# Optimization experiments

Measured on AMD Instinct MI355X. Metric: run time of the kernel, lower is better.

## Reference

```python
import jax, jax.numpy as jnp
import numpy as np

H, S, B, R, IN, NN, OP = 512, 256, 32, 16, 4, 16, 6
NEG = -1.0e12


def setup_inputs() -> dict:
    key = jax.random.key(0)
    ks = jax.random.split(key, 40)
    f32 = jnp.float32
    inp = {}
    inp["node_emb"] = jax.random.normal(ks[0], (B, 1, H), f32)
    inp["left"] = jax.random.normal(ks[1], (B, 1, H), f32)
    inp["encoder_outputs"] = jax.random.normal(ks[2], (S, B, H), f32)
    inp["num_pades"] = jax.random.normal(ks[3], (B, NN, H), f32)
    inp["formula_scores"] = jax.random.normal(ks[4], (R, H), f32)
    inp["has_left"] = jax.random.bernoulli(ks[5], 0.5, (B,))
    lengths = jax.random.randint(ks[6], (B,), S // 2, S + 1)
    inp["seq_mask"] = jnp.arange(S)[None, :] >= lengths[:, None]
    nlen = jax.random.randint(ks[7], (B,), (IN + NN) // 2, IN + NN + 1)
    inp["mask_nums"] = jnp.arange(IN + NN)[None, :] >= nlen[:, None]
    sc = 0.04  # init scale for weights
    def w(i, shape):
        return jax.random.normal(ks[i], shape, f32) * sc
    inp["embedding_weight"] = jax.random.normal(ks[8], (1, IN, H), f32)
    inp["Wcl"] = w(9, (H, H));    inp["bcl"] = jnp.zeros((H,), f32)
    inp["Wclg"] = w(10, (H, H));  inp["bclg"] = jnp.zeros((H,), f32)
    inp["Wcr"] = w(11, (2 * H, H));  inp["bcr"] = jnp.zeros((H,), f32)
    inp["Wcrg"] = w(12, (2 * H, H)); inp["bcrg"] = jnp.zeros((H,), f32)
    inp["Wops"] = w(13, (2 * H, OP)); inp["bops"] = jnp.zeros((OP,), f32)
    inp["Wattn"] = w(14, (2 * H, H)); inp["battn"] = jnp.zeros((H,), f32)
    inp["wattn_s"] = w(15, (H,));     inp["battn_s"] = jnp.zeros((), f32)
    inp["Wfattn"] = w(16, (2 * H, H)); inp["bfattn"] = jnp.zeros((H,), f32)
    inp["wfattn_s"] = w(17, (H,));     inp["bfattn_s"] = jnp.zeros((), f32)
    inp["Wscore"] = w(18, (3 * H, H)); inp["bscore"] = jnp.zeros((H,), f32)
    inp["wscore_s"] = w(19, (H,))  # Score.score has no bias
    inp["Wfp1"] = w(20, (H, H));   inp["bfp1"] = jnp.zeros((H,), f32)
    inp["Wfp2"] = w(21, (H,));     inp["bfp2"] = jnp.zeros((), f32)
    return inp


def _forward(node_emb, left, has_left, encoder_outputs, num_pades, seq_mask,
             mask_nums, formula_scores, embedding_weight, Wcl, bcl, Wclg, bclg,
             Wcr, bcr, Wcrg, bcrg, Wops, bops, Wattn, battn, wattn_s, battn_s,
             Wfattn, bfattn, wfattn_s, bfattn_s, Wscore, bscore, wscore_s,
             Wfp1, bfp1, Wfp2, bfp2):
    # gated left/right node update (dropout = identity, eval mode)
    c = node_emb                                            # [B,1,H]
    lc = jnp.concatenate([left, c], axis=-1)                # [B,1,2H]
    out_l = jnp.tanh(c @ Wcl + bcl) * jax.nn.sigmoid(c @ Wclg + bclg)
    out_r = jnp.tanh(lc @ Wcr + bcr) * jax.nn.sigmoid(lc @ Wcrg + bcrg)
    current_node = jnp.where(has_left[:, None, None], out_r, out_l)  # [B,1,H]
    # TreeAttn(current_node, encoder_outputs): additive attention over S
    Wh, We = Wattn[:H], Wattn[H:]
    feat = jnp.tanh(current_node[:, 0][None] @ Wh + encoder_outputs @ We + battn)  # [S,B,H]
    en = (feat @ wattn_s + battn_s).T                       # [B,S]
    en = jnp.where(seq_mask, NEG, en)
    current_attn = jax.nn.softmax(en, axis=1)[:, None, :]   # [B,1,S]
    eo_b = jnp.transpose(encoder_outputs, (1, 0, 2))        # [B,S,H]
    current_context = current_attn @ eo_b                   # [B,1,H]
    # embedding table = learned constants + numbers from the problem
    emb_w = jnp.concatenate(
        [jnp.broadcast_to(embedding_weight, (node_emb.shape[0], IN, H)), num_pades], axis=1)  # [B,IN+NN,H]
    leaf_input = jnp.concatenate([current_node, current_context], axis=2)[:, 0]  # [B,2H]
    # FormulaAttn: additive attention of each formula over all tokens
    Wfe, Wff = Wfattn[:H], Wfattn[H:]
    ffeat = jnp.tanh(encoder_outputs[None] @ Wfe
                     + (formula_scores @ Wff)[:, None, None, :] + bfattn)  # [R,S,B,H]
    fen = jnp.transpose(ffeat @ wfattn_s + bfattn_s, (2, 0, 1))            # [B,R,S]
    fen = jnp.where(seq_mask[:, None, :], NEG, fen)
    formulas_attn = jax.nn.softmax(fen, axis=-1)            # [B,R,S]
    formulas_context = (formulas_attn + 0.2 * current_attn) @ eo_b         # [B,R,H]
    formula_feat = jnp.tanh(formulas_context @ Wfp1 + bfp1)
    formula_prob = jax.nn.softmax(formula_feat @ Wfp2 + bfp2, axis=-1)     # [B,R]
    # Score over candidate number embeddings
    N = IN + NN
    hid = jnp.broadcast_to(leaf_input[:, None, :], (leaf_input.shape[0], N, 2 * H))
    ein = jnp.concatenate([hid, emb_w], axis=-1)            # [B,N,3H]
    ns = jnp.tanh(ein @ Wscore + bscore) @ wscore_s         # [B,N]
    num_score = jnp.where(mask_nums, NEG, ns)
    op = leaf_input @ Wops + bops                           # [B,OP]
    return (num_score, op, current_node, current_context, emb_w, formula_prob)


def reference(node_emb, left, has_left, encoder_outputs, num_pades, seq_mask,
              mask_nums, formula_scores, embedding_weight, Wcl, bcl, Wclg, bclg,
              Wcr, bcr, Wcrg, bcrg, Wops, bops, Wattn, battn, wattn_s, battn_s,
              Wfattn, bfattn, wfattn_s, bfattn_s, Wscore, bscore, wscore_s,
              Wfp1, bfp1, Wfp2, bfp2):
    return _forward(node_emb, left, has_left, encoder_outputs, num_pades,
                    seq_mask, mask_nums, formula_scores, embedding_weight,
                    Wcl, bcl, Wclg, bclg, Wcr, bcr, Wcrg, bcrg, Wops, bops,
                    Wattn, battn, wattn_s, battn_s, Wfattn, bfattn, wfattn_s,
                    bfattn_s, Wscore, bscore, wscore_s, Wfp1, bfp1, Wfp2, bfp2)
```

## Files before the change

### kernel.cpp

```cpp
#include <hip/hip_runtime.h>
#include <hip/hip_bf16.h>
#include <stdint.h>

#define H 512
#define S 256
#define B 32
#define R 16
#define NEG -1000000000000.0f

typedef unsigned short u16;
typedef short short8 __attribute__((ext_vector_type(8)));
typedef float f32x4 __attribute__((ext_vector_type(4)));

__device__ __forceinline__ float bf2f(u16 u) {
  unsigned int v = ((unsigned int)u) << 16;
  float f; __builtin_memcpy(&f, &v, 4); return f;
}
__device__ __forceinline__ u16 f2u(float x) {
  __hip_bfloat16 h = __float2bfloat16(x);
  u16 u; __builtin_memcpy(&u, &h, 2); return u;
}
__device__ __forceinline__ float ftanh(float x) {
  float e = __expf(2.f * x);
  return 1.f - 2.f * __builtin_amdgcn_rcpf(e + 1.f);
}
__device__ __forceinline__ float ptanh(float x) {
  float xc = fminf(4.f, fmaxf(-4.f, x));
  float x2 = xc * xc;
  float num = xc * (945.f + x2 * (105.f + x2));
  float den = 945.f + x2 * (420.f + 15.f * x2);
  return num * __builtin_amdgcn_rcpf(den);
}
__device__ __forceinline__ float fsig(float x) {
  return __builtin_amdgcn_rcpf(1.f + __expf(-x));
}
__device__ __forceinline__ void gload16(const void* g, void* l) {
  __builtin_amdgcn_global_load_lds(
      (const __attribute__((address_space(1))) unsigned int*)g,
      (__attribute__((address_space(3))) unsigned int*)l, 16, 0, 0);
}

__device__ __forceinline__ void trans_tile(const float* __restrict__ src, int nb, int k0,
                                           u16* __restrict__ dst, int n0, int Krows,
                                           float (*tile)[65], int t) {
  #pragma unroll
  for (int it = 0; it < 16; ++it) {
    int f = it * 256 + t; int r = f >> 6, c = f & 63;
    tile[r][c] = src[(size_t)(k0 + r) * 512 + nb + c];
  }
  __syncthreads();
  #pragma unroll
  for (int it = 0; it < 16; ++it) {
    int f = it * 256 + t; int r = f >> 6, c = f & 63;
    dst[(size_t)(n0 + r) * Krows + k0 + c] = f2u(tile[c][r]);
  }
}

__global__ __launch_bounds__(256) void k_prep1(
    const float* __restrict__ enc, u16* __restrict__ encb,
    const float* __restrict__ Wattn, const float* __restrict__ Wfattn, u16* __restrict__ Wt,
    const float* __restrict__ Wscore, u16* __restrict__ Wt2a, u16* __restrict__ Wt2b,
    const float* __restrict__ Wfp1, u16* __restrict__ Wt3,
    u16* __restrict__ Wt4,
    const float* __restrict__ node_emb, const float* __restrict__ left,
    const int* __restrict__ has_left,
    const float* __restrict__ Wcl, const float* __restrict__ Wclg,
    const float* __restrict__ Wcr, const float* __restrict__ Wcrg,
    float* __restrict__ gp1, float* __restrict__ gp2,
    const float* __restrict__ emb_w, const float* __restrict__ num_pades,
    float* __restrict__ out_embw, u16* __restrict__ embb, u16* __restrict__ leafb) {
  __shared__ float tile[64][65];
  __shared__ float x[128];
  int id = blockIdx.x, t = threadIdx.x;
  if (id < 2048) {
    int i = (id * 256 + t) * 8;
    float4 a = *(const float4*)(enc + i);
    float4 b = *(const float4*)(enc + i + 4);
    short8 o;
    o[0] = (short)f2u(a.x); o[1] = (short)f2u(a.y); o[2] = (short)f2u(a.z); o[3] = (short)f2u(a.w);
    o[4] = (short)f2u(b.x); o[5] = (short)f2u(b.y); o[6] = (short)f2u(b.z); o[7] = (short)f2u(b.w);
    *(short8*)(encb + i) = o;
  } else if (id < 2176) {
    int f = id - 2048; int gx = f & 15, gy = f >> 4;
    int n0 = gx * 64, k0 = gy * 64;
    const float* src = (n0 < 512) ? (Wattn + 512 * 512) : Wfattn;
    int nb = (n0 < 512) ? n0 : n0 - 512;
    trans_tile(src, nb, k0, Wt, n0, 512, tile, t);
  } else if (id < 2240) {
    int f = id - 2176; int gx = f & 7, gy = f >> 3;
    trans_tile(Wscore + 1024 * 512, gx * 64, gy * 64, Wt2a, gx * 64, 512, tile, t);
  } else if (id < 2368) {
    int f = id - 2240; int gx = f & 7, gy = f >> 3;
    trans_tile(Wscore, gx * 64, gy * 64, Wt2b, gx * 64, 1024, tile, t);
  } else if (id < 2432) {
    int f = id - 2368; int gx = f & 7, gy = f >> 3;
    trans_tile(Wfp1, gx * 64, gy * 64, Wt3, gx * 64, 512, tile, t);
  } else if (id < 2560) {
    int f = id - 2432; int gx = f & 15, gy = f >> 4;
    int n0 = gx * 64, k0 = gy * 64;
    const float* src = (n0 < 512) ? Wattn : (Wfattn + 512 * 512);
    int nb = (n0 < 512) ? n0 : n0 - 512;
    trans_tile(src, nb, k0, Wt4, n0, 512, tile, t);
  } else if (id < 2816) {
    int f = id - 2560;
    int b = f >> 3, kc = f & 7;
    int hl = has_left[b];
    int k0 = kc * 128;
    float* o1 = gp1 + ((size_t)b * 8 + kc) * 512;
    float* o2 = gp2 + ((size_t)b * 8 + kc) * 512;
    if (!hl && kc >= 4) { o1[t] = 0.f; o1[t + 256] = 0.f; o2[t] = 0.f; o2[t + 256] = 0.f; return; }
    if (t < 128) {
      int k = k0 + t;
      x[t] = hl ? (k < 512 ? left[b * 512 + k] : node_emb[b * 512 + k - 512])
                : node_emb[b * 512 + k];
    }
    __syncthreads();
    const float* W1 = hl ? Wcr : Wcl;
    const float* W2 = hl ? Wcrg : Wclg;
    float a1 = 0.f, a2 = 0.f, a3 = 0.f, a4 = 0.f;
    for (int kk = 0; kk < 128; ++kk) {
      float xv = x[kk];
      const float* w1r = W1 + (size_t)(k0 + kk) * 512;
      const float* w2r = W2 + (size_t)(k0 + kk) * 512;
      a1 += xv * w1r[t]; a2 += xv * w1r[t + 256];
      a3 += xv * w2r[t]; a4 += xv * w2r[t + 256];
    }
    o1[t] = a1; o1[t + 256] = a2; o2[t] = a3; o2[t + 256] = a4;
  } else if (id < 3136) {
    int f = id - 2816;
    #pragma unroll
    for (int rr = 0; rr < 2; ++rr) {
      int row = f * 2 + rr;
      int n = row % 20, b = row / 20;
      #pragma unroll
      for (int i = 0; i < 2; ++i) {
        int h = t + 256 * i;
        float v = (n < 4) ? emb_w[n * 512 + h] : num_pades[((size_t)b * 16 + n - 4) * 512 + h];
        out_embw[(size_t)row * 512 + h] = v;
        embb[(size_t)row * 512 + h] = f2u(v);
      }
    }
  } else {
    int f = id - 3136;
    int base = 32 * 1024 + (f * 256 + t) * 16;
    short8 z8 = {0,0,0,0,0,0,0,0};
    *(short8*)(leafb + base) = z8;
    *(short8*)(leafb + base + 8) = z8;
  }
}

template <int FM, int FN>
__device__ __forceinline__ void gemm_body(
    const u16* __restrict__ A, const u16* __restrict__ Bt,
    u16* __restrict__ C16, float* __restrict__ C32,
    int lda, int ldb, int ldc, int ksteps,
    int bm, int bn, int kbase, long zoff,
    u16* As, u16* Bs) {
  constexpr int BM = FM * 32, BN = FN * 32;
  const int tid = threadIdx.x;
  const int lane = tid & 63;
  const int wid = tid >> 6;
  const int wr = (wid >> 1) * (FM * 16);
  const int wc = (wid & 1) * (FN * 16);
  f32x4 acc[FM][FN];
  #pragma unroll
  for (int m = 0; m < FM; ++m)
    #pragma unroll
    for (int n = 0; n < FN; ++n)
      #pragma unroll
      for (int q = 0; q < 4; ++q) acc[m][n][q] = 0.f;

  const int kb = (lane >> 4) * 8;
  const int rr = lane & 15;
  for (int ks = 0; ks < ksteps; ++ks) {
    int k0 = kbase + ks * 32;
    #pragma unroll
    for (int it = 0; it < BM / 64; ++it) {
      int c = it * 256 + tid;
      gload16(A + (size_t)(bm + (c >> 2)) * lda + k0 + (c & 3) * 8, As + c * 8);
    }
    #pragma unroll
    for (int it = 0; it < BN / 64; ++it) {
      int c = it * 256 + tid;
      gload16(Bt + (size_t)(bn + (c >> 2)) * ldb + k0 + (c & 3) * 8, Bs + c * 8);
    }
    __syncthreads();
    short8 af[FM], bf[FN];
    #pragma unroll
    for (int m = 0; m < FM; ++m)
      af[m] = *(const short8*)(As + (wr + m * 16 + rr) * 32 + kb);
    #pragma unroll
    for (int n = 0; n < FN; ++n)
      bf[n] = *(const short8*)(Bs + (wc + n * 16 + rr) * 32 + kb);
    #pragma unroll
    for (int m = 0; m < FM; ++m)
      #pragma unroll
      for (int n = 0; n < FN; ++n)
        acc[m][n] = __builtin_amdgcn_mfma_f32_16x16x32_bf16(af[m], bf[n], acc[m][n], 0, 0, 0);
    __syncthreads();
  }
  int r0 = (lane >> 4) * 4, cc = lane & 15;
  #pragma unroll
  for (int m = 0; m < FM; ++m)
    #pragma unroll
    for (int n = 0; n < FN; ++n)
      #pragma unroll
      for (int q = 0; q < 4; ++q) {
        long row = bm + wr + m * 16 + r0 + q;
        long col = bn + wc + n * 16 + cc;
        if (C16) C16[zoff + row * ldc + col] = f2u(acc[m][n][q]);
        else     C32[zoff + row * ldc + col] = acc[m][n][q];
      }
}

__global__ __launch_bounds__(256) void k_g1(
    const u16* __restrict__ encb, const u16* __restrict__ Wt, u16* __restrict__ EW,
    const u16* __restrict__ cnfs, const u16* __restrict__ Wt4, float* __restrict__ CWFW,
    const u16* __restrict__ embb, const u16* __restrict__ Wt2a, float* __restrict__ Tep) {
  __shared__ u16 As[128 * 32];
  __shared__ u16 Bs[128 * 32];
  int q = blockIdx.x;
  if (q < 512) {
    int x = q & 63, y = q >> 6;
    gemm_body<4, 4>(encb, Wt, EW, nullptr, 512, 512, 1024, 16, x * 128, y * 128, 0, 0, As, Bs);
  } else if (q < 520) {
    int y = q - 512;
    gemm_body<4, 4>(cnfs, Wt4, nullptr, CWFW, 512, 512, 1024, 16, 0, y * 128, 0, 0, As, Bs);
  } else {
    int q2 = q - 520;
    int x = q2 % 10, y = (q2 / 10) % 8, z = q2 / 80;
    gemm_body<2, 2>(embb, Wt2a, nullptr, Tep, 512, 512, 512, 4,
                    x * 64, y * 64, z * 4 * 32, (long)z * 327680, As, Bs);
  }
}

__global__ __launch_bounds__(256) void k_tt(
    const u16* __restrict__ leafb, const u16* __restrict__ Wt2b, float* __restrict__ Tlp,
    const u16* __restrict__ fctxb, const u16* __restrict__ Wt3, float* __restrict__ T3p,
    const float* __restrict__ leaf, const float* __restrict__ Wops,
    const float* __restrict__ bops, float* __restrict__ out_op) {
  __shared__ u16 As[64 * 32];
  __shared__ u16 Bs[64 * 32];
  __shared__ float red[4];
  int q = blockIdx.x;
  if (q < 32) {
    int y = q % 8, z = q / 8;
    gemm_body<2, 2>(leafb, Wt2b, nullptr, Tlp, 1024, 1024, 512, 8,
                    0, y * 64, z * 8 * 32, (long)z * 32768, As, Bs);
  } else if (q < 288) {
    int q2 = q - 32;
    int x = q2 % 8, y = (q2 / 8) % 8, z = q2 / 64;
    gemm_body<2, 2>(fctxb, Wt3, nullptr, T3p, 512, 512, 512, 4,
                    x * 64, y * 64, z * 4 * 32, (long)z * 262144, As, Bs);
  } else {
    int f = q - 288; int o = f % 6, b = f / 6;
    int t = threadIdx.x, w = t >> 6, lane = t & 63;
    float acc = 0.f;
    #pragma unroll
    for (int i = 0; i < 4; ++i) {
      int k = t + 256 * i;
      acc += leaf[b * 1024 + k] * Wops[(size_t)k * 6 + o];
    }
    for (int off = 32; off >= 1; off >>= 1) acc += __shfl_down(acc, off);
    if (lane == 0) red[w] = acc;
    __syncthreads();
    if (t == 0) out_op[b * 6 + o] = red[0] + red[1] + red[2] + red[3] + bops[o];
  }
}

__global__ __launch_bounds__(256) void k_p2(
    const float* __restrict__ gp1, const float* __restrict__ gp2,
    const int* __restrict__ has_left,
    const float* __restrict__ bcl, const float* __restrict__ bclg,
    const float* __restrict__ bcr, const float* __restrict__ bcrg,
    const float* __restrict__ fs,
    float* __restrict__ cur_node, float* __restrict__ out_cn, u16* __restrict__ cnfs) {
  int id = blockIdx.x, t = threadIdx.x;
  if (id < 32) {
    int b = id, hl = has_left[b];
    #pragma unroll
    for (int i = 0; i < 2; ++i) {
      int h = t + 256 * i;
      float s1 = 0.f, s2 = 0.f;
      #pragma unroll
      for (int c = 0; c < 8; ++c) {
        s1 += gp1[((size_t)b * 8 + c) * 512 + h];
        s2 += gp2[((size_t)b * 8 + c) * 512 + h];
      }
      float v = ftanh(s1 + (hl ? bcr[h] : bcl[h])) * fsig(s2 + (hl ? bcrg[h] : bclg[h]));
      cur_node[b * 512 + h] = v;
      out_cn[b * 512 + h] = v;
      cnfs[b * 512 + h] = f2u(v);
    }
  } else if (id < 48) {
    int r = id - 32;
    #pragma unroll
    for (int i = 0; i < 2; ++i) {
      int h = t + 256 * i;
      cnfs[id * 512 + h] = f2u(fs[r * 512 + h]);
    }
  } else {
    #pragma unroll
    for (int i = 0; i < 2; ++i) cnfs[id * 512 + t + 256 * i] = 0;
  }
}

__global__ __launch_bounds__(256) void k_enfen(
    const u16* __restrict__ EW, const float* __restrict__ CWFW,
    const float* __restrict__ battn, const float* __restrict__ bfattn,
    const float* __restrict__ wattn_s, const float* __restrict__ battn_s,
    const float* __restrict__ wfattn_s, const float* __restrict__ bfattn_s,
    const int* __restrict__ seq_mask, float* __restrict__ en, float* __restrict__ fen) {
  __shared__ float sFW[16 * 512];
  __shared__ float swf[512], swa[512], scw[512];
  int bid = blockIdx.x;
  int b = bid >> 5;
  int s0 = (bid & 31) * 8;
  int t = threadIdx.x;
  #pragma unroll
  for (int q = 0; q < 32; ++q) {
    int flat = q * 256 + t;
    int r = flat >> 9, h = flat & 511;
    sFW[flat] = CWFW[(size_t)(32 + r) * 1024 + 512 + h] + bfattn[h];
  }
  swf[t] = wfattn_s[t]; swf[256 + t] = wfattn_s[256 + t];
  swa[t] = wattn_s[t];  swa[256 + t] = wattn_s[256 + t];
  scw[t] = CWFW[(size_t)b * 1024 + t] + battn[t];
  scw[256 + t] = CWFW[(size_t)b * 1024 + 256 + t] + battn[256 + t];
  __syncthreads();
  int w = t >> 6, lane = t & 63;
  float wav[8], wfv[8], cwv[8];
  #pragma unroll
  for (int i = 0; i < 8; ++i) {
    int h = lane + 64 * i;
    wav[i] = swa[h]; wfv[i] = swf[h]; cwv[i] = scw[h];
  }
  #pragma unroll
  for (int si = 0; si < 2; ++si) {
    int s = s0 + w * 2 + si;
    int msk = seq_mask[b * 256 + s];
    if (msk) {
      if (lane == 0) {
        en[b * 256 + s] = NEG;
        for (int r = 0; r < 16; ++r) fen[((size_t)b * 16 + r) * 256 + s] = NEG;
      }
      continue;
    }
    const u16* ew = EW + (size_t)(s * 32 + b) * 1024;
    float ewf[8];
    float accE = 0.f;
    #pragma unroll
    for (int i = 0; i < 8; ++i) {
      int h = lane + 64 * i;
      accE += ptanh(cwv[i] + bf2f(ew[h])) * wav[i];
      ewf[i] = bf2f(ew[512 + h]);
    }
    for (int o = 32; o >= 1; o >>= 1) accE += __shfl_down(accE, o);
    if (lane == 0) en[b * 256 + s] = accE + battn_s[0];
    for (int r = 0; r < 16; ++r) {
      float a = 0.f;
      #pragma unroll
      for (int i = 0; i < 8; ++i) {
        int h = lane + 64 * i;
        a += ptanh(sFW[r * 512 + h] + ewf[i]) * wfv[i];
      }
      for (int o = 32; o >= 1; o >>= 1) a += __shfl_down(a, o);
      if (lane == 0) fen[((size_t)b * 16 + r) * 256 + s] = a + bfattn_s[0];
    }
  }
}

__global__ __launch_bounds__(512) void k_ctxall(
    const float* __restrict__ en, const float* __restrict__ fen,
    const u16* __restrict__ encb, const float* __restrict__ cur_node,
    float* __restrict__ out_ctx, float* __restrict__ leaf, u16* __restrict__ fctxb,
    u16* __restrict__ leafb) {
  int br = blockIdx.x;
  int b = br / 9, k = br % 9;
  int t = threadIdx.x;
  __shared__ float red[512];
  __shared__ float sa0[256], sa1[256];
  float xe = (t < 256) ? en[b * 256 + t] : NEG;
  red[t] = xe; __syncthreads();
  for (int o = 256; o > 0; o >>= 1) { if (t < o) red[t] = fmaxf(red[t], red[t + o]); __syncthreads(); }
  float m = red[0]; __syncthreads();
  float ee = (t < 256) ? __expf(xe - m) : 0.f;
  red[t] = ee; __syncthreads();
  for (int o = 256; o > 0; o >>= 1) { if (t < o) red[t] += red[t + o]; __syncthreads(); }
  float attn_v = ee / red[0];
  __syncthreads();
  if (k < 8) {
    #pragma unroll
    for (int p = 0; p < 2; ++p) {
      int j = k + p * 8;
      float xf = (t < 256) ? fen[((size_t)b * 16 + j) * 256 + t] : NEG;
      red[t] = xf; __syncthreads();
      for (int o = 256; o > 0; o >>= 1) { if (t < o) red[t] = fmaxf(red[t], red[t + o]); __syncthreads(); }
      float mf = red[0]; __syncthreads();
      float ef = (t < 256) ? __expf(xf - mf) : 0.f;
      red[t] = ef; __syncthreads();
      for (int o = 256; o > 0; o >>= 1) { if (t < o) red[t] += red[t + o]; __syncthreads(); }
      float coef = ef / red[0] + 0.2f * attn_v;
      __syncthreads();
      if (t < 256) { if (p == 0) sa0[t] = coef; else sa1[t] = coef; }
    }
    __syncthreads();
    int h = t;
    float acc0 = 0.f, acc1 = 0.f;
    #pragma unroll 8
    for (int s = 0; s < 256; ++s) {
      float ev = bf2f(encb[((size_t)s * 32 + b) * 512 + h]);
      acc0 += sa0[s] * ev;
      acc1 += sa1[s] * ev;
    }
    fctxb[((size_t)b * 16 + k) * 512 + h] = f2u(acc0);
    fctxb[((size_t)b * 16 + k + 8) * 512 + h] = f2u(acc1);
  } else {
    if (t < 256) sa0[t] = attn_v;
    __syncthreads();
    int h = t;
    float acc = 0.f;
    #pragma unroll 8
    for (int s = 0; s < 256; ++s)
      acc += sa0[s] * bf2f(encb[((size_t)s * 32 + b) * 512 + h]);
    float cn = cur_node[b * 512 + h];
    out_ctx[b * 512 + h] = acc;
    leaf[b * 1024 + 512 + h] = acc;
    leaf[b * 1024 + h] = cn;
    leafb[b * 1024 + h] = f2u(cn);
    leafb[b * 1024 + 512 + h] = f2u(acc);
  }
}

__global__ __launch_bounds__(256) void k_epi(
    const float* __restrict__ Tep, const float* __restrict__ Tlp,
    const float* __restrict__ bscore,
    const float* __restrict__ wscore_s, const int* __restrict__ mask_nums,
    float* __restrict__ out_ns,
    const float* __restrict__ T3p, const float* __restrict__ bfp1,
    const float* __restrict__ Wfp2, const float* __restrict__ bfp2,
    float* __restrict__ out_fp) {
  int id = blockIdx.x, t = threadIdx.x;
  int w = t >> 6, lane = t & 63;
  __shared__ float red[16];
  if (id < 640) {
    int row = id;
    int b = row / 20;
    float acc = 0.f;
    #pragma unroll
    for (int i = 0; i < 2; ++i) {
      int h = t + 256 * i;
      float tv = bscore[h];
      #pragma unroll
      for (int z = 0; z < 4; ++z) tv += Tep[(size_t)z * 327680 + (size_t)row * 512 + h];
      #pragma unroll
      for (int z = 0; z < 4; ++z) tv += Tlp[(size_t)z * 32768 + (size_t)b * 512 + h];
      acc += ftanh(tv) * wscore_s[h];
    }
    for (int o = 32; o >= 1; o >>= 1) acc += __shfl_down(acc, o);
    if (lane == 0) red[w] = acc;
    __syncthreads();
    if (t == 0) out_ns[row] = mask_nums[row] ? NEG : (red[0] + red[1] + red[2] + red[3]);
  } else {
    int b = id - 640;
    #pragma unroll
    for (int j2 = 0; j2 < 4; ++j2) {
      int j = w * 4 + j2;
      int row = b * 16 + j;
      float acc = 0.f;
      #pragma unroll
      for (int i = 0; i < 8; ++i) {
        int h = lane + 64 * i;
        float v = bfp1[h];
        #pragma unroll
        for (int z = 0; z < 4; ++z) v += T3p[(size_t)z * 262144 + (size_t)row * 512 + h];
        acc += ftanh(v) * Wfp2[h];
      }
      for (int o = 32; o >= 1; o >>= 1) acc += __shfl_down(acc, o);
      if (lane == 0) red[j] = acc + bfp2[0];
    }
    __syncthreads();
    if (t < 16) {
      float xx = red[t];
      float mm = xx;
      for (int o = 8; o >= 1; o >>= 1) mm = fmaxf(mm, __shfl_xor(mm, o, 16));
      float e = __expf(xx - mm);
      float s2 = e;
      for (int o = 8; o >= 1; o >>= 1) s2 += __shfl_xor(s2, o, 16);
      out_fp[b * 16 + t] = e / s2;
    }
  }
}

extern "C" void kernel_launch(void* const* d_in, const int* in_sizes, int n_in,
                              void* d_out, int out_size, void* d_ws, size_t ws_size,
                              hipStream_t stream) {
  const float* node_emb  = (const float*)d_in[0];
  const float* left      = (const float*)d_in[1];
  const float* enc       = (const float*)d_in[2];
  const float* num_pades = (const float*)d_in[3];
  const float* fs        = (const float*)d_in[4];
  const int*   has_left  = (const int*)d_in[5];
  const int*   seq_mask  = (const int*)d_in[6];
  const int*   mask_nums = (const int*)d_in[7];
  const float* emb_w     = (const float*)d_in[8];
  const float* Wcl  = (const float*)d_in[9];
  const float* bcl  = (const float*)d_in[10];
  const float* Wclg = (const float*)d_in[11];
  const float* bclg = (const float*)d_in[12];
  const float* Wcr  = (const float*)d_in[13];
  const float* bcr  = (const float*)d_in[14];
  const float* Wcrg = (const float*)d_in[15];
  const float* bcrg = (const float*)d_in[16];
  const float* Wops = (const float*)d_in[17];
  const float* bops = (const float*)d_in[18];
  const float* Wattn   = (const float*)d_in[19];
  const float* battn   = (const float*)d_in[20];
  const float* wattn_s = (const float*)d_in[21];
  const float* battn_s = (const float*)d_in[22];
  const float* Wfattn   = (const float*)d_in[23];
  const float* bfattn   = (const float*)d_in[24];
  const float* wfattn_s = (const float*)d_in[25];
  const float* bfattn_s = (const float*)d_in[26];
  const float* Wscore   = (const float*)d_in[27];
  const float* bscore   = (const float*)d_in[28];
  const float* wscore_s = (const float*)d_in[29];
  const float* Wfp1 = (const float*)d_in[30];
  const float* bfp1 = (const float*)d_in[31];
  const float* Wfp2 = (const float*)d_in[32];
  const float* bfp2 = (const float*)d_in[33];

  float* out = (float*)d_out;
  float* out_ns   = out + 0;
  float* out_op   = out + 640;
  float* out_cn   = out + 832;
  float* out_ctx  = out + 17216;
  float* out_embw = out + 33600;
  float* out_fp   = out + 361280;

  uint8_t* wsb = (uint8_t*)d_ws;
  u16*   encb = (u16*)(wsb + 0);
  u16*   Wt   = (u16*)(wsb + 8388608);
  u16*   Wt2a = (u16*)(wsb + 9437184);
  u16*   Wt2b = (u16*)(wsb + 9961472);
  u16*   Wt3  = (u16*)(wsb + 11010048);
  u16*   Wt4  = (u16*)(wsb + 11534336);
  u16*   EW   = (u16*)(wsb + 12582912);
  u16*   embb = (u16*)(wsb + 29360128);
  u16*   leafb= (u16*)(wsb + 30015488);
  u16*   cnfs = (u16*)(wsb + 30146560);
  float* CWFW = (float*)(wsb + 30277632);
  float* Tep  = (float*)(wsb + 30801920);
  float* Tlp  = (float*)(wsb + 36044800);
  float* T3p  = (float*)(wsb + 36569088);
  float* fb   = (float*)(wsb + 40763392);
  float* cur_node = fb + 0;
  float* en   = fb + 16384;
  float* fen  = fb + 24576;
  float* leaf = fb + 155648;
  u16*   fctxb= (u16*)(fb + 188416);
  float* gp1  = fb + 319488;
  float* gp2  = fb + 450560;

  k_prep1<<<3144, 256, 0, stream>>>(enc, encb, Wattn, Wfattn, Wt, Wscore, Wt2a, Wt2b,
                                    Wfp1, Wt3, Wt4,
                                    node_emb, left, has_left, Wcl, Wclg, Wcr, Wcrg,
                                    gp1, gp2, emb_w, num_pades, out_embw, embb, leafb);
  k_p2<<<128, 256, 0, stream>>>(gp1, gp2, has_left, bcl, bclg, bcr, bcrg, fs,
                                cur_node, out_cn, cnfs);
  k_g1<<<840, 256, 0, stream>>>(encb, Wt, EW, cnfs, Wt4, CWFW, embb, Wt2a, Tep);
  k_enfen<<<1024, 256, 0, stream>>>(EW, CWFW, battn, bfattn, wattn_s, battn_s,
                                    wfattn_s, bfattn_s, seq_mask, en, fen);
  k_ctxall<<<288, 512, 0, stream>>>(en, fen, encb, cur_node, out_ctx, leaf, fctxb, leafb);
  k_tt<<<480, 256, 0, stream>>>(leafb, Wt2b, Tlp, fctxb, Wt3, T3p,
                                leaf, Wops, bops, out_op);
  k_epi<<<672, 256, 0, stream>>>(Tep, Tlp, bscore, wscore_s, mask_nums, out_ns,
                                 T3p, bfp1, Wfp2, bfp2, out_fp);
}
```

Baseline: 104.8 us.

## Add batch-major bf16 encoder copy, interleave two seq positions, halve Tep split-K

The prep kernel now also writes a batch-major [B,S,H] bf16 copy of the encoder outputs. The context kernel reads this copy so each block streams contiguous rows instead of rows strided by batch. The energy kernel processes its two sequence positions together, sharing shared-memory loads and shuffle reductions, and exits early when both are masked. The embedding-score GEMM goes from 4 to 2 split-K chunks, which drops 160 blocks and the extra partial-sum reads in the epilogue. In exchange there is an extra 8 MB write in prep and fewer blocks available to parallelise that GEMM.

```diff
diff --git a/kernel.cpp b/kernel.cpp
--- a/kernel.cpp
+++ b/kernel.cpp
@@ -57,7 +57,7 @@
 }
 
 __global__ __launch_bounds__(256) void k_prep1(
-    const float* __restrict__ enc, u16* __restrict__ encb,
+    const float* __restrict__ enc, u16* __restrict__ encb, u16* __restrict__ encc,
     const float* __restrict__ Wattn, const float* __restrict__ Wfattn, u16* __restrict__ Wt,
     const float* __restrict__ Wscore, u16* __restrict__ Wt2a, u16* __restrict__ Wt2b,
     const float* __restrict__ Wfp1, u16* __restrict__ Wt3,
@@ -75,11 +75,13 @@
   if (id < 2048) {
     int i = (id * 256 + t) * 8;
     float4 a = *(const float4*)(enc + i);
-    float4 b = *(const float4*)(enc + i + 4);
+    float4 b4 = *(const float4*)(enc + i + 4);
     short8 o;
     o[0] = (short)f2u(a.x); o[1] = (short)f2u(a.y); o[2] = (short)f2u(a.z); o[3] = (short)f2u(a.w);
-    o[4] = (short)f2u(b.x); o[5] = (short)f2u(b.y); o[6] = (short)f2u(b.z); o[7] = (short)f2u(b.w);
+    o[4] = (short)f2u(b4.x); o[5] = (short)f2u(b4.y); o[6] = (short)f2u(b4.z); o[7] = (short)f2u(b4.w);
     *(short8*)(encb + i) = o;
+    int s = i >> 14, b = (i >> 9) & 31, h = i & 511;
+    *(short8*)(encc + (((size_t)b << 8) + s) * 512 + h) = o;
   } else if (id < 2176) {
     int f = id - 2048; int gx = f & 15, gy = f >> 4;
     int n0 = gx * 64, k0 = gy * 64;
@@ -229,8 +231,8 @@
   } else {
     int q2 = q - 520;
     int x = q2 % 10, y = (q2 / 10) % 8, z = q2 / 80;
-    gemm_body<2, 2>(embb, Wt2a, nullptr, Tep, 512, 512, 512, 4,
-                    x * 64, y * 64, z * 4 * 32, (long)z * 327680, As, Bs);
+    gemm_body<2, 2>(embb, Wt2a, nullptr, Tep, 512, 512, 512, 8,
+                    x * 64, y * 64, z * 8 * 32, (long)z * 327680, As, Bs);
   }
 }
 
@@ -329,50 +331,63 @@
   scw[256 + t] = CWFW[(size_t)b * 1024 + 256 + t] + battn[256 + t];
   __syncthreads();
   int w = t >> 6, lane = t & 63;
-  float wav[8], wfv[8], cwv[8];
+  int sA = s0 + w * 2, sB = sA + 1;
+  int mA = seq_mask[b * 256 + sA], mB = seq_mask[b * 256 + sB];
+  if (mA && mB) {
+    if (lane == 0) {
+      en[b * 256 + sA] = NEG; en[b * 256 + sB] = NEG;
+      for (int r = 0; r < 16; ++r) {
+        fen[((size_t)b * 16 + r) * 256 + sA] = NEG;
+        fen[((size_t)b * 16 + r) * 256 + sB] = NEG;
+      }
+    }
+    return;
+  }
+  const u16* ewA = EW + (size_t)(sA * 32 + b) * 1024;
+  const u16* ewB = EW + (size_t)(sB * 32 + b) * 1024;
+  float ewfA[8], ewfB[8], wfv[8];
+  float accA = 0.f, accB = 0.f;
   #pragma unroll
   for (int i = 0; i < 8; ++i) {
     int h = lane + 64 * i;
-    wav[i] = swa[h]; wfv[i] = swf[h]; cwv[i] = scw[h];
-  }
-  #pragma unroll
-  for (int si = 0; si < 2; ++si) {
-    int s = s0 + w * 2 + si;
-    int msk = seq_mask[b * 256 + s];
-    if (msk) {
-      if (lane == 0) {
-        en[b * 256 + s] = NEG;
-        for (int r = 0; r < 16; ++r) fen[((size_t)b * 16 + r) * 256 + s] = NEG;
-      }
-      continue;
-    }
-    const u16* ew = EW + (size_t)(s * 32 + b) * 1024;
-    float ewf[8];
-    float accE = 0.f;
+    float cw = scw[h], wa = swa[h];
+    accA += ptanh(cw + bf2f(ewA[h])) * wa;
+    accB += ptanh(cw + bf2f(ewB[h])) * wa;
+    ewfA[i] = bf2f(ewA[512 + h]);
+    ewfB[i] = bf2f(ewB[512 + h]);
+    wfv[i] = swf[h];
+  }
+  for (int o = 32; o >= 1; o >>= 1) {
+    accA += __shfl_down(accA, o);
+    accB += __shfl_down(accB, o);
+  }
+  if (lane == 0) {
+    en[b * 256 + sA] = mA ? NEG : (accA + battn_s[0]);
+    en[b * 256 + sB] = mB ? NEG : (accB + battn_s[0]);
+  }
+  for (int r = 0; r < 16; ++r) {
+    float a0 = 0.f, a1 = 0.f;
     #pragma unroll
     for (int i = 0; i < 8; ++i) {
       int h = lane + 64 * i;
-      accE += ptanh(cwv[i] + bf2f(ew[h])) * wav[i];
-      ewf[i] = bf2f(ew[512 + h]);
-    }
-    for (int o = 32; o >= 1; o >>= 1) accE += __shfl_down(accE, o);
-    if (lane == 0) en[b * 256 + s] = accE + battn_s[0];
-    for (int r = 0; r < 16; ++r) {
-      float a = 0.f;
-      #pragma unroll
-      for (int i = 0; i < 8; ++i) {
-        int h = lane + 64 * i;
-        a += ptanh(sFW[r * 512 + h] + ewf[i]) * wfv[i];
-      }
-      for (int o = 32; o >= 1; o >>= 1) a += __shfl_down(a, o);
-      if (lane == 0) fen[((size_t)b * 16 + r) * 256 + s] = a + bfattn_s[0];
+      float fwv = sFW[r * 512 + h];
+      a0 += ptanh(fwv + ewfA[i]) * wfv[i];
+      a1 += ptanh(fwv + ewfB[i]) * wfv[i];
+    }
+    for (int o = 32; o >= 1; o >>= 1) {
+      a0 += __shfl_down(a0, o);
+      a1 += __shfl_down(a1, o);
+    }
+    if (lane == 0) {
+      fen[((size_t)b * 16 + r) * 256 + sA] = mA ? NEG : (a0 + bfattn_s[0]);
+      fen[((size_t)b * 16 + r) * 256 + sB] = mB ? NEG : (a1 + bfattn_s[0]);
     }
   }
 }
 
 __global__ __launch_bounds__(512) void k_ctxall(
     const float* __restrict__ en, const float* __restrict__ fen,
-    const u16* __restrict__ encb, const float* __restrict__ cur_node,
+    const u16* __restrict__ encc, const float* __restrict__ cur_node,
     float* __restrict__ out_ctx, float* __restrict__ leaf, u16* __restrict__ fctxb,
     u16* __restrict__ leafb) {
   int br = blockIdx.x;
@@ -389,6 +404,7 @@
   for (int o = 256; o > 0; o >>= 1) { if (t < o) red[t] += red[t + o]; __syncthreads(); }
   float attn_v = ee / red[0];
   __syncthreads();
+  const u16* eb = encc + (size_t)b * 131072;
   if (k < 8) {
     #pragma unroll
     for (int p = 0; p < 2; ++p) {
@@ -409,7 +425,7 @@
     float acc0 = 0.f, acc1 = 0.f;
     #pragma unroll 8
     for (int s = 0; s < 256; ++s) {
-      float ev = bf2f(encb[((size_t)s * 32 + b) * 512 + h]);
+      float ev = bf2f(eb[(size_t)s * 512 + h]);
       acc0 += sa0[s] * ev;
       acc1 += sa1[s] * ev;
     }
@@ -422,7 +438,7 @@
     float acc = 0.f;
     #pragma unroll 8
     for (int s = 0; s < 256; ++s)
-      acc += sa0[s] * bf2f(encb[((size_t)s * 32 + b) * 512 + h]);
+      acc += sa0[s] * bf2f(eb[(size_t)s * 512 + h]);
     float cn = cur_node[b * 512 + h];
     out_ctx[b * 512 + h] = acc;
     leaf[b * 1024 + 512 + h] = acc;
@@ -452,7 +468,7 @@
       int h = t + 256 * i;
       float tv = bscore[h];
       #pragma unroll
-      for (int z = 0; z < 4; ++z) tv += Tep[(size_t)z * 327680 + (size_t)row * 512 + h];
+      for (int z = 0; z < 2; ++z) tv += Tep[(size_t)z * 327680 + (size_t)row * 512 + h];
       #pragma unroll
       for (int z = 0; z < 4; ++z) tv += Tlp[(size_t)z * 32768 + (size_t)b * 512 + h];
       acc += ftanh(tv) * wscore_s[h];
@@ -561,17 +577,18 @@
   u16*   fctxb= (u16*)(fb + 188416);
   float* gp1  = fb + 319488;
   float* gp2  = fb + 450560;
-
-  k_prep1<<<3144, 256, 0, stream>>>(enc, encb, Wattn, Wfattn, Wt, Wscore, Wt2a, Wt2b,
+  u16*   encc = (u16*)(wsb + 45088768);
+
+  k_prep1<<<3144, 256, 0, stream>>>(enc, encb, encc, Wattn, Wfattn, Wt, Wscore, Wt2a, Wt2b,
                                     Wfp1, Wt3, Wt4,
                                     node_emb, left, has_left, Wcl, Wclg, Wcr, Wcrg,
                                     gp1, gp2, emb_w, num_pades, out_embw, embb, leafb);
   k_p2<<<128, 256, 0, stream>>>(gp1, gp2, has_left, bcl, bclg, bcr, bcrg, fs,
                                 cur_node, out_cn, cnfs);
-  k_g1<<<840, 256, 0, stream>>>(encb, Wt, EW, cnfs, Wt4, CWFW, embb, Wt2a, Tep);
+  k_g1<<<680, 256, 0, stream>>>(encb, Wt, EW, cnfs, Wt4, CWFW, embb, Wt2a, Tep);
   k_enfen<<<1024, 256, 0, stream>>>(EW, CWFW, battn, bfattn, wattn_s, battn_s,
                                     wfattn_s, bfattn_s, seq_mask, en, fen);
-  k_ctxall<<<288, 512, 0, stream>>>(en, fen, encb, cur_node, out_ctx, leaf, fctxb, leafb);
+  k_ctxall<<<288, 512, 0, stream>>>(en, fen, encc, cur_node, out_ctx, leaf, fctxb, leafb);
   k_tt<<<480, 256, 0, stream>>>(leafb, Wt2b, Tlp, fctxb, Wt3, T3p,
                                 leaf, Wops, bops, out_op);
   k_epi<<<672, 256, 0, stream>>>(Tep, Tlp, bscore, wscore_s, mask_nums, out_ns,
```

Measured after the change: 99.27 us (median of 2 runs). -5.3%, faster.
